# Performance work log

Measured on AMD Instinct MI355X. Metric: run time of the kernel, lower is better.

## Reference

```python
import jax, jax.numpy as jnp
import numpy as np

B, L, D, H, K_DELAYS = 8, 2048, 512, 8, 8
DH = D // H


def setup_inputs() -> dict:
    key = jax.random.key(0)
    ks = jax.random.split(key, 6)
    def lin_w(k):
        return 0.02 * jax.random.normal(k, (D, D), jnp.float32)
    return {
        "x_q":  jax.random.normal(ks[0], (B, L, D), jnp.float32),
        "x_kv": jax.random.normal(ks[1], (B, L, D), jnp.float32),
        "Wq": lin_w(ks[2]), "bq": jnp.zeros((D,), jnp.float32),
        "Wk": lin_w(ks[3]), "bk": jnp.zeros((D,), jnp.float32),
        "Wv": lin_w(ks[4]), "bv": jnp.zeros((D,), jnp.float32),
        "Wo": lin_w(ks[5]), "bo": jnp.zeros((D,), jnp.float32),
    }


def reference(x_q, x_kv, Wq, bq, Wk, bk, Wv, bv, Wo, bo):
    Bx, Lx, Dx = x_q.shape

    def proj(x, W, b):  # torch Linear: x @ W.T + b, then split heads -> [B,H,L,dh]
        return (x @ W.T + b).reshape(Bx, Lx, H, DH).transpose(0, 2, 1, 3)

    q = proj(x_q, Wq, bq)
    k = proj(x_kv, Wk, bk)
    v = proj(x_kv, Wv, bv)

    # FFT-based autocorrelation over the time axis (axis=2)
    qz = q - q.mean(axis=2, keepdims=True)
    kz = k - k.mean(axis=2, keepdims=True)
    Qf = jnp.fft.rfft(qz, axis=2)
    Kf = jnp.fft.rfft(kz, axis=2)
    corr = jnp.fft.irfft(Qf * jnp.conj(Kf), n=Lx, axis=2).mean(axis=-1)  # [B,H,L]
    # torch expands corr to [B,H,Lq,Lk] then means over Lq -> identical to corr
    score = corr

    K = min(K_DELAYS, Lx)
    vals, idx = jax.lax.top_k(score, K)                    # [B,H,K]
    w = vals / (vals.sum(axis=-1, keepdims=True) + 1e-12)
    w = jax.lax.stop_gradient(w)                           # .detach() in torch

    # circular shift by -delay == gather at (t + delay) mod L
    t = jnp.arange(Lx)
    pos = (t[None, None, None, :] + idx[..., None]) % Lx   # [B,H,K,L]
    v_sh = jnp.take_along_axis(v[:, :, None, :, :], pos[..., None], axis=3)  # [B,H,K,L,dh]
    out = jnp.einsum('bhk,bhkld->bhld', w, v_sh)           # weighted sum over delays

    out = out.transpose(0, 2, 1, 3).reshape(Bx, Lx, Dx)
    return out @ Wo.T + bo
```

## Files before the change

kernel.cpp:

```cpp
#include <hip/hip_runtime.h>
#include <math.h>

#define BB 8
#define LL 2048
#define DD 512
#define HH 8
#define DHH 64
#define KD 8
#define MM (BB*LL)

typedef _Float16 f16x2 __attribute__((ext_vector_type(2)));
typedef _Float16 f16x4 __attribute__((ext_vector_type(4)));
typedef _Float16 f16x8 __attribute__((ext_vector_type(8)));
typedef float    f32x4 __attribute__((ext_vector_type(4)));

__device__ inline void cvt8(const float* __restrict__ s, _Float16* hp, _Float16* lp) {
    const float4 a = *(const float4*)s;
    const float4 b = *(const float4*)(s + 4);
    const float v[8] = {a.x, a.y, a.z, a.w, b.x, b.y, b.z, b.w};
    f16x8 hi, lo;
#pragma unroll
    for (int j = 0; j < 8; j++) {
        const _Float16 h = (_Float16)v[j];
        hi[j] = h;
        lo[j] = (_Float16)((v[j] - (float)h) * 512.0f);
    }
    *(f16x8*)hp = hi;
    if (lp) *(f16x8*)lp = lo;
}

__global__ __launch_bounds__(256) void prep_all(const float* __restrict__ xq,
                                                const float* __restrict__ xkv,
                                                const float* __restrict__ Wq, const float* __restrict__ Wk,
                                                const float* __restrict__ Wv, const float* __restrict__ Wo,
                                                _Float16* __restrict__ Xq_h, _Float16* __restrict__ Xq_l,
                                                _Float16* __restrict__ Xkv_h, _Float16* __restrict__ Xkv_l,
                                                _Float16* __restrict__ Wq_h, _Float16* __restrict__ Wq_l,
                                                _Float16* __restrict__ Wk_h, _Float16* __restrict__ Wk_l,
                                                _Float16* __restrict__ Wv_h, _Float16* __restrict__ Wo_h) {
    const int bid = blockIdx.x;
    if (bid < 8192) {
        const int g = bid * 256 + threadIdx.x;
        const int which = g >> 20;
        const size_t idx = (size_t)(g & 1048575) * 8;
        const float* src = which ? xkv : xq;
        _Float16* dh = which ? Xkv_h : Xq_h;
        _Float16* dl = which ? Xkv_l : Xq_l;
        cvt8(src + idx, dh + idx, dl + idx);
    } else {
        const int g = (bid - 8192) * 256 + threadIdx.x;
        const int which = g >> 15;
        const size_t idx = (size_t)(g & 32767) * 8;
        if (which == 0)      cvt8(Wq + idx, Wq_h + idx, Wq_l + idx);
        else if (which == 1) cvt8(Wk + idx, Wk_h + idx, Wk_l + idx);
        else if (which == 2) cvt8(Wv + idx, Wv_h + idx, nullptr);
        else                 cvt8(Wo + idx, Wo_h + idx, nullptr);
    }
}

template<int NPROD, int MODE>
__device__ __forceinline__ void gemm_body(const _Float16* __restrict__ Ag,
                                          const _Float16* __restrict__ Al_g,
                                          const _Float16* __restrict__ Bg,
                                          const _Float16* __restrict__ Bl_g,
                                          const float* __restrict__ bias,
                                          void* __restrict__ Cv,
                                          _Float16* lds, int l0) {
    _Float16* Ah = lds;
    _Float16* Bh = lds + 5120;
    _Float16* Al = (NPROD == 3) ? lds + 10240 : lds;
    _Float16* Bl = (NPROD == 3) ? lds + 15360 : lds;

    const int t  = threadIdx.x;
    const int m0 = (((l0 >> 5) << 3) | (l0 & 7)) * 128;
    const int n0 = ((l0 >> 3) & 3) * 128;

    const int lrow = t >> 2;
    const int lcol = (t & 3) * 8;
    const int wave = t >> 6;
    const int lane = t & 63;
    const int wm   = (wave >> 1) * 64;
    const int wn   = (wave & 1) * 64;
    const int lm   = lane & 15;
    const int quad = lane >> 4;

    f32x4 acc0[4][4] = {};
    f32x4 acc1[4][4] = {};

    f16x8 pa[2], pb[2], pal[2], pbl[2];
#pragma unroll
    for (int p = 0; p < 2; p++) {
        pa[p] = *(const f16x8*)(Ag + (size_t)(m0 + p * 64 + lrow) * 512 + lcol);
        pb[p] = *(const f16x8*)(Bg + (size_t)(n0 + p * 64 + lrow) * 512 + lcol);
        if (NPROD == 3) {
            pal[p] = *(const f16x8*)(Al_g + (size_t)(m0 + p * 64 + lrow) * 512 + lcol);
            pbl[p] = *(const f16x8*)(Bl_g + (size_t)(n0 + p * 64 + lrow) * 512 + lcol);
        }
    }

    for (int k0 = 0; k0 < 512; k0 += 32) {
        __syncthreads();
#pragma unroll
        for (int p = 0; p < 2; p++) {
            const int row = p * 64 + lrow;
            *(f16x8*)&Ah[row * 40 + lcol] = pa[p];
            *(f16x8*)&Bh[row * 40 + lcol] = pb[p];
            if (NPROD == 3) {
                *(f16x8*)&Al[row * 40 + lcol] = pal[p];
                *(f16x8*)&Bl[row * 40 + lcol] = pbl[p];
            }
        }
        __syncthreads();

        if (k0 + 32 < 512) {
            const int kn = k0 + 32;
#pragma unroll
            for (int p = 0; p < 2; p++) {
                pa[p] = *(const f16x8*)(Ag + (size_t)(m0 + p * 64 + lrow) * 512 + kn + lcol);
                pb[p] = *(const f16x8*)(Bg + (size_t)(n0 + p * 64 + lrow) * 512 + kn + lcol);
                if (NPROD == 3) {
                    pal[p] = *(const f16x8*)(Al_g + (size_t)(m0 + p * 64 + lrow) * 512 + kn + lcol);
                    pbl[p] = *(const f16x8*)(Bl_g + (size_t)(n0 + p * 64 + lrow) * 512 + kn + lcol);
                }
            }
        }

        f16x8 afh[4], bf[4];
#pragma unroll
        for (int mt = 0; mt < 4; mt++)
            afh[mt] = *(f16x8*)&Ah[(wm + mt * 16 + lm) * 40 + quad * 8];
#pragma unroll
        for (int nt = 0; nt < 4; nt++)
            bf[nt] = *(f16x8*)&Bh[(wn + nt * 16 + lm) * 40 + quad * 8];

#pragma unroll
        for (int mt = 0; mt < 4; mt++)
#pragma unroll
            for (int nt = 0; nt < 4; nt++)
                acc0[mt][nt] = __builtin_amdgcn_mfma_f32_16x16x32_f16(afh[mt], bf[nt], acc0[mt][nt], 0, 0, 0);

        if (NPROD == 3) {
            f16x8 afl[4];
#pragma unroll
            for (int mt = 0; mt < 4; mt++)
                afl[mt] = *(f16x8*)&Al[(wm + mt * 16 + lm) * 40 + quad * 8];
#pragma unroll
            for (int mt = 0; mt < 4; mt++)
#pragma unroll
                for (int nt = 0; nt < 4; nt++)
                    acc1[mt][nt] = __builtin_amdgcn_mfma_f32_16x16x32_f16(afl[mt], bf[nt], acc1[mt][nt], 0, 0, 0);
#pragma unroll
            for (int nt = 0; nt < 4; nt++)
                bf[nt] = *(f16x8*)&Bl[(wn + nt * 16 + lm) * 40 + quad * 8];
#pragma unroll
            for (int mt = 0; mt < 4; mt++)
#pragma unroll
                for (int nt = 0; nt < 4; nt++)
                    acc1[mt][nt] = __builtin_amdgcn_mfma_f32_16x16x32_f16(afh[mt], bf[nt], acc1[mt][nt], 0, 0, 0);
        }
    }

#pragma unroll
    for (int mt = 0; mt < 4; mt++) {
#pragma unroll
        for (int nt = 0; nt < 4; nt++) {
            const int n = n0 + wn + nt * 16 + lm;
            const float bv = bias[n];
            float val[4];
#pragma unroll
            for (int r = 0; r < 4; r++) {
                val[r] = acc0[mt][nt][r] + bv;
                if (NPROD == 3) val[r] += acc1[mt][nt][r] * (1.0f / 512.0f);
            }
            const int mbase = m0 + wm + mt * 16 + quad * 4;
            const int b_idx = mbase >> 11;
            const int lbase = mbase & 2047;
            if (MODE == 0) {
                float* C = (float*)Cv;
#pragma unroll
                for (int r = 0; r < 4; r++) C[(size_t)(mbase + r) * 512 + n] = val[r];
            } else if (MODE == 1) {
                float* C = (float*)Cv;
                float4 pv = make_float4(val[0], val[1], val[2], val[3]);
                *(float4*)&C[((size_t)(b_idx * 512 + n)) * 2048 + lbase] = pv;
            } else {
                _Float16* C = (_Float16*)Cv;
#pragma unroll
                for (int r = 0; r < 4; r++)
                    C[(size_t)b_idx * 1048576 + (size_t)(n >> 6) * 131072
                      + (size_t)(lbase + r) * 64 + (n & 63)] = (_Float16)val[r];
            }
        }
    }
}

__global__ __launch_bounds__(256, 2) void gemm_qk(const _Float16* __restrict__ A0h, const _Float16* __restrict__ A0l,
                                                  const _Float16* __restrict__ B0h, const _Float16* __restrict__ B0l,
                                                  const float* __restrict__ bias0, float* __restrict__ C0,
                                                  const _Float16* __restrict__ A1h, const _Float16* __restrict__ A1l,
                                                  const _Float16* __restrict__ B1h, const _Float16* __restrict__ B1l,
                                                  const float* __restrict__ bias1, float* __restrict__ C1) {
    __shared__ __align__(16) _Float16 lds[20480];
    const int prob = blockIdx.x >> 9;
    const int l0   = blockIdx.x & 511;
    if (prob == 0)
        gemm_body<3, 1>(A0h, A0l, B0h, B0l, bias0, C0, lds, l0);
    else
        gemm_body<3, 1>(A1h, A1l, B1h, B1l, bias1, C1, lds, l0);
}

__global__ __launch_bounds__(256, 2) void gemm_v(const _Float16* __restrict__ Ah_g,
                                                 const _Float16* __restrict__ Bh_g,
                                                 const float* __restrict__ bias,
                                                 _Float16* __restrict__ C) {
    __shared__ __align__(16) _Float16 lds[10240];
    gemm_body<1, 2>(Ah_g, Ah_g, Bh_g, Bh_g, bias, C, lds, blockIdx.x);
}

__global__ __launch_bounds__(256, 2) void gemm_o(const _Float16* __restrict__ Ah_g,
                                                 const _Float16* __restrict__ Bh_g,
                                                 const float* __restrict__ bias,
                                                 float* __restrict__ C) {
    __shared__ __align__(16) _Float16 lds[10240];
    gemm_body<1, 0>(Ah_g, Ah_g, Bh_g, Bh_g, bias, C, lds, blockIdx.x);
}

#define PAD3(i) ((i) + ((i) >> 3))

__device__ inline float2 cmul2(float2 a, float2 w) {
    return make_float2(a.x * w.x - a.y * w.y, a.x * w.y + a.y * w.x);
}
__device__ inline float2 cadd2(float2 a, float2 b) { return make_float2(a.x + b.x, a.y + b.y); }
__device__ inline float2 csub2(float2 a, float2 b) { return make_float2(a.x - b.x, a.y - b.y); }

__global__ __launch_bounds__(256) void fft_fwd(const float* __restrict__ qT,
                                               const float* __restrict__ kT,
                                               float* __restrict__ specP) {
    const int blk  = blockIdx.x;
    const int bh   = blk >> 4;
    const int part = blk & 15;
    const int t    = threadIdx.x;
    __shared__ float2 Zs[2304];
    __shared__ float2 Wt[1024];

#pragma unroll
    for (int s = 0; s < 4; s++) {
        const int j = t + s * 256;
        float sv, cv;
        __sincosf(2.0f * (float)M_PI * (float)j / 2048.0f, &sv, &cv);
        Wt[j] = make_float2(cv, -sv);
    }

    float2 pacc[8];
#pragma unroll
    for (int s = 0; s < 8; s++) pacc[s] = make_float2(0.0f, 0.0f);

    const int low5 = t & 31, hi3 = t >> 5;
    const int low2 = t & 3,  hi6 = t >> 2;

    for (int j4 = 0; j4 < 4; j4++) {
        const int seq = bh * 64 + part * 4 + j4;
        const float* qp = qT + (size_t)seq * 2048;
        const float* kp = kT + (size_t)seq * 2048;
        float2 z[8];
#pragma unroll
        for (int s = 0; s < 8; s++) z[s] = make_float2(qp[t + 256 * s], kp[t + 256 * s]);
        __syncthreads();

#pragma unroll
        for (int sp = 0; sp < 4; sp++) {
            float2 u = z[sp], v = z[sp + 4];
            z[sp]     = cadd2(u, v);
            z[sp + 4] = cmul2(csub2(u, v), Wt[t + 256 * sp]);
        }
#pragma unroll
        for (int base = 0; base < 8; base += 4)
#pragma unroll
            for (int q2 = 0; q2 < 2; q2++) {
                float2 u = z[base + q2], v = z[base + q2 + 2];
                z[base + q2]     = cadd2(u, v);
                z[base + q2 + 2] = cmul2(csub2(u, v), Wt[2 * (t + 256 * q2)]);
            }
        {
            const float2 w = Wt[4 * t];
#pragma unroll
            for (int e = 0; e < 8; e += 2) {
                float2 u = z[e], v = z[e + 1];
                z[e]     = cadd2(u, v);
                z[e + 1] = cmul2(csub2(u, v), w);
            }
        }

#pragma unroll
        for (int s = 0; s < 8; s++) Zs[PAD3(t + 256 * s)] = z[s];
        __syncthreads();
#pragma unroll
        for (int s = 0; s < 8; s++) z[s] = Zs[PAD3(low5 + 32 * s + 256 * hi3)];

#pragma unroll
        for (int sp = 0; sp < 4; sp++) {
            float2 u = z[sp], v = z[sp + 4];
            z[sp]     = cadd2(u, v);
            z[sp + 4] = cmul2(csub2(u, v), Wt[8 * (low5 + 32 * sp)]);
        }
#pragma unroll
        for (int base = 0; base < 8; base += 4)
#pragma unroll
            for (int q2 = 0; q2 < 2; q2++) {
                float2 u = z[base + q2], v = z[base + q2 + 2];
                z[base + q2]     = cadd2(u, v);
                z[base + q2 + 2] = cmul2(csub2(u, v), Wt[16 * (low5 + 32 * q2)]);
            }
        {
            const float2 w = Wt[32 * low5];
#pragma unroll
            for (int e = 0; e < 8; e += 2) {
                float2 u = z[e], v = z[e + 1];
                z[e]     = cadd2(u, v);
                z[e + 1] = cmul2(csub2(u, v), w);
            }
        }

#pragma unroll
        for (int s = 0; s < 8; s++) Zs[PAD3(low5 + 32 * s + 256 * hi3)] = z[s];
        __syncthreads();
#pragma unroll
        for (int s = 0; s < 8; s++) z[s] = Zs[PAD3(low2 + 4 * s + 32 * hi6)];

#pragma unroll
        for (int sp = 0; sp < 4; sp++) {
            float2 u = z[sp], v = z[sp + 4];
            z[sp]     = cadd2(u, v);
            z[sp + 4] = cmul2(csub2(u, v), Wt[64 * (low2 + 4 * sp)]);
        }
#pragma unroll
        for (int base = 0; base < 8; base += 4)
#pragma unroll
            for (int q2 = 0; q2 < 2; q2++) {
                float2 u = z[base + q2], v = z[base + q2 + 2];
                z[base + q2]     = cadd2(u, v);
                z[base + q2 + 2] = cmul2(csub2(u, v), Wt[128 * (low2 + 4 * q2)]);
            }
        {
            const float2 w = Wt[256 * low2];
#pragma unroll
            for (int e = 0; e < 8; e += 2) {
                float2 u = z[e], v = z[e + 1];
                z[e]     = cadd2(u, v);
                z[e + 1] = cmul2(csub2(u, v), w);
            }
        }

#pragma unroll
        for (int s = 0; s < 8; s++) Zs[PAD3(low2 + 4 * s + 32 * hi6)] = z[s];
        __syncthreads();
#pragma unroll
        for (int s = 0; s < 8; s++) z[s] = Zs[PAD3(8 * t + s)];

#pragma unroll
        for (int base = 0; base < 8; base += 4) {
            {
                float2 u = z[base], v = z[base + 2];
                z[base]     = cadd2(u, v);
                z[base + 2] = csub2(u, v);
            }
            {
                float2 u = z[base + 1], v = z[base + 3];
                float2 d = csub2(u, v);
                z[base + 1] = cadd2(u, v);
                z[base + 3] = make_float2(d.y, -d.x);
            }
        }
#pragma unroll
        for (int e = 0; e < 8; e += 2) {
            float2 u = z[e], v = z[e + 1];
            z[e]     = cadd2(u, v);
            z[e + 1] = csub2(u, v);
        }

#pragma unroll
        for (int s = 0; s < 8; s++) Zs[PAD3(8 * t + s)] = z[s];
        __syncthreads();

#pragma unroll
        for (int s = 0; s < 8; s++) {
            const int p  = t + 256 * s;
            const int f  = (int)(__brev((unsigned)p) >> 21);
            const int fm = (2048 - f) & 2047;
            const int p2 = (int)(__brev((unsigned)fm) >> 21);
            const float2 zf = Zs[PAD3(p)];
            const float2 zm = Zs[PAD3(p2)];
            const float qr = 0.5f * (zf.x + zm.x);
            const float qi = 0.5f * (zf.y - zm.y);
            const float kr = 0.5f * (zf.y + zm.y);
            const float ki = 0.5f * (zm.x - zf.x);
            if (f != 0) {
                pacc[s].x += qr * kr + qi * ki;
                pacc[s].y += qi * kr - qr * ki;
            }
        }
    }

    float2* outp = (float2*)specP + (size_t)blk * 2048;
#pragma unroll
    for (int s = 0; s < 8; s++) outp[t + 256 * s] = pacc[s];
}

__device__ inline void build_twiddle(float2* Wt, int tid, float sign) {
#pragma unroll
    for (int s = 0; s < 4; s++) {
        const int j = tid + s * 256;
        const float a = 2.0f * (float)M_PI * (float)j / 2048.0f;
        float sv, cv;
        __sincosf(a, &sv, &cv);
        Wt[j] = make_float2(cv, sign * sv);
    }
}

__device__ inline void fft2048_stages(float2* Z, const float2* Wt, int tid) {
    for (int st = 0; st < 11; st++) {
        const int half = 1 << st;
        const int shift = 10 - st;
#pragma unroll
        for (int r = 0; r < 4; r++) {
            const int m   = tid + r * 256;
            const int grp = m >> st;
            const int pos = m & (half - 1);
            const int i0  = (grp << (st + 1)) + pos;
            const int i1  = i0 + half;
            const float2 w = Wt[pos << shift];
            const float2 a = Z[i0];
            const float2 b = Z[i1];
            const float tr = b.x * w.x - b.y * w.y;
            const float ti = b.x * w.y + b.y * w.x;
            Z[i0] = make_float2(a.x + tr, a.y + ti);
            Z[i1] = make_float2(a.x - tr, a.y - ti);
        }
        __syncthreads();
    }
}

__global__ __launch_bounds__(256) void fft_inv_topk(const float* __restrict__ specP,
                                                    int* __restrict__ delays,
                                                    float* __restrict__ weights) {
    const int bh  = blockIdx.x;
    const int tid = threadIdx.x;
    __shared__ float2 Z[2048];
    __shared__ float2 Wt[1024];
    __shared__ float  corrS[2048];
    __shared__ float  rv[256];
    __shared__ int    ri[256];
    __shared__ float  vals[KD];
    __shared__ int    inds[KD];

    build_twiddle(Wt, tid, +1.0f);

    const float2* sp = (const float2*)specP + (size_t)bh * 16 * 2048;
#pragma unroll
    for (int s = 0; s < 8; s++) {
        const int p = tid + s * 256;
        float2 acc = make_float2(0.0f, 0.0f);
#pragma unroll
        for (int part = 0; part < 16; part++) {
            const float2 v = sp[part * 2048 + p];
            acc.x += v.x; acc.y += v.y;
        }
        Z[p] = acc;
    }
    __syncthreads();
    fft2048_stages(Z, Wt, tid);

    const float scale = 1.0f / (2048.0f * 64.0f);
#pragma unroll
    for (int s = 0; s < 8; s++) {
        const int i = tid + s * 256;
        corrS[i] = Z[i].x * scale;
    }
    __syncthreads();

    for (int k = 0; k < KD; k++) {
        float best = -1e30f;
        int   bi   = 1 << 30;
        for (int i = tid; i < 2048; i += 256) {
            const float v = corrS[i];
            if (v > best || (v == best && i < bi)) { best = v; bi = i; }
        }
        rv[tid] = best;
        ri[tid] = bi;
        __syncthreads();
        for (int off = 128; off > 0; off >>= 1) {
            if (tid < off) {
                const float v2 = rv[tid + off];
                const int   i2 = ri[tid + off];
                if (v2 > rv[tid] || (v2 == rv[tid] && i2 < ri[tid])) {
                    rv[tid] = v2; ri[tid] = i2;
                }
            }
            __syncthreads();
        }
        if (tid == 0) {
            vals[k] = rv[0];
            inds[k] = ri[0];
            corrS[ri[0]] = -1e30f;
        }
        __syncthreads();
    }

    if (tid == 0) {
        float sum = 0.0f;
        for (int k = 0; k < KD; k++) sum += vals[k];
        const float inv = 1.0f / (sum + 1e-12f);
        for (int k = 0; k < KD; k++) {
            weights[bh * KD + k] = vals[k] * inv;
            delays[bh * KD + k]  = inds[k];
        }
    }
}

__global__ __launch_bounds__(256) void gather_ws(const _Float16* __restrict__ v,
                                                 const int* __restrict__ delays,
                                                 const float* __restrict__ weights,
                                                 _Float16* __restrict__ outb) {
    const int gp = blockIdx.x * 256 + threadIdx.x;
    const int c8 = gp & 63;
    const int m  = gp >> 6;
    const int l  = m & 2047;
    const int b  = m >> 11;
    const int ch = c8 * 8;
    const int h  = ch >> 6;
    const int dh = ch & 63;
    const int bh = b * 8 + h;

    const _Float16* vb = v + (size_t)bh * 131072;
    float a[8] = {};
#pragma unroll
    for (int k = 0; k < KD; k++) {
        const int   d = delays[bh * KD + k];
        const float w = weights[bh * KD + k];
        const int   p = (l + d) & 2047;
        const f16x8 pv = *(const f16x8*)&vb[p * 64 + dh];
#pragma unroll
        for (int j = 0; j < 8; j++) a[j] = fmaf(w, (float)pv[j], a[j]);
    }
    f16x8 ov;
#pragma unroll
    for (int j = 0; j < 8; j++) ov[j] = (_Float16)a[j];
    *(f16x8*)&outb[(size_t)m * 512 + ch] = ov;
}

extern "C" void kernel_launch(void* const* d_in, const int* in_sizes, int n_in,
                              void* d_out, int out_size, void* d_ws, size_t ws_size,
                              hipStream_t stream) {
    const float* x_q  = (const float*)d_in[0];
    const float* x_kv = (const float*)d_in[1];
    const float* Wq   = (const float*)d_in[2];
    const float* bq   = (const float*)d_in[3];
    const float* Wk   = (const float*)d_in[4];
    const float* bk   = (const float*)d_in[5];
    const float* Wv   = (const float*)d_in[6];
    const float* bv   = (const float*)d_in[7];
    const float* Wo   = (const float*)d_in[8];
    const float* bo   = (const float*)d_in[9];
    float* out = (float*)d_out;

    char* ws = (char*)d_ws;
    _Float16* Xq_h  = (_Float16*)(ws + 0);
    _Float16* Xq_l  = (_Float16*)(ws + 16777216);
    _Float16* Xkv_h = (_Float16*)(ws + 33554432);
    _Float16* Xkv_l = (_Float16*)(ws + 50331648);
    _Float16* Wq_h  = (_Float16*)(ws + 67108864);
    _Float16* Wq_l  = (_Float16*)(ws + 67633152);
    _Float16* Wk_h  = (_Float16*)(ws + 68157440);
    _Float16* Wk_l  = (_Float16*)(ws + 68681728);
    _Float16* Wv_h  = (_Float16*)(ws + 69206016);
    _Float16* Wo_h  = (_Float16*)(ws + 69730304);
    int*      dely  = (int*)    (ws + 70254592);
    float*    wgt   = (float*)  (ws + 70256640);
    float*    kf32  = (float*)  (ws + 75497472);
    float*    specP = (float*)  (ws + 50331648);
    _Float16* vh    = (_Float16*)(ws + 0);
    _Float16* gbuf  = (_Float16*)(ws + 16777216);
    float*    qf32  = (float*)d_out;

    (void)0;

    dim3 blk(256);

    prep_all<<<dim3(8704), blk, 0, stream>>>(x_q, x_kv, Wq, Wk, Wv, Wo,
                                             Xq_h, Xq_l, Xkv_h, Xkv_l,
                                             Wq_h, Wq_l, Wk_h, Wk_l, Wv_h, Wo_h);

    gemm_qk<<<dim3(512), blk, 0, stream>>>(Xq_h, Xq_l, Wq_h, Wq_l, bq, qf32,
                                           Xq_h, Xq_l, Wq_h, Wq_l, bq, qf32);
    {
        float* kf32_ = (float*)(ws + 0);
        gemm_qk<<<dim3(512), blk, 0, stream>>>(Xkv_h, Xkv_l, Wk_h, Wk_l, bk, kf32_,
                                               Xkv_h, Xkv_l, Wk_h, Wk_l, bk, kf32_);
    }

    fft_fwd<<<dim3(1024), blk, 0, stream>>>(qf32, (float*)(ws + 0), specP);
    fft_inv_topk<<<dim3(BB * HH), blk, 0, stream>>>(specP, dely, wgt);

    gemm_v<<<dim3(512), blk, 0, stream>>>(Xkv_h, Wv_h, bv, vh);

    gather_ws<<<dim3(4096), blk, 0, stream>>>(vh, dely, wgt, gbuf);

    gemm_o<<<dim3(512), blk, 0, stream>>>(gbuf, Wo_h, bo, out);
}
```

Measured before the change: 302.3 us.

## Merge inverse FFT/top-k into V-projection GEMM launch and use wave-shuffle top-k

Combines the 64-block inverse-FFT/top-k kernel with the V-projection GEMM into one 576-block launch: the first 64 blocks do the FFT path and the rest do GEMM tiles, so the small, latency-bound FFT work overlaps with the GEMM instead of running alone on a mostly idle GPU. The top-k selection now keeps correlation values in registers and reduces with wavefront shuffles plus a 4-entry cross-wave step, replacing the shared-memory tree reduction that needed many barriers per iteration. Shared memory is a single raw buffer sized for the larger of the two uses, which may reduce occupancy for the GEMM blocks.

```diff
diff --git a/kernel.cpp b/kernel.cpp
--- a/kernel.cpp
+++ b/kernel.cpp
@@ -209,14 +209,6 @@
         gemm_body<3, 1>(A1h, A1l, B1h, B1l, bias1, C1, lds, l0);
 }
 
-__global__ __launch_bounds__(256, 2) void gemm_v(const _Float16* __restrict__ Ah_g,
-                                                 const _Float16* __restrict__ Bh_g,
-                                                 const float* __restrict__ bias,
-                                                 _Float16* __restrict__ C) {
-    __shared__ __align__(16) _Float16 lds[10240];
-    gemm_body<1, 2>(Ah_g, Ah_g, Bh_g, Bh_g, bias, C, lds, blockIdx.x);
-}
-
 __global__ __launch_bounds__(256, 2) void gemm_o(const _Float16* __restrict__ Ah_g,
                                                  const _Float16* __restrict__ Bh_g,
                                                  const float* __restrict__ bias,
@@ -440,18 +432,27 @@
     }
 }
 
-__global__ __launch_bounds__(256) void fft_inv_topk(const float* __restrict__ specP,
-                                                    int* __restrict__ delays,
-                                                    float* __restrict__ weights) {
-    const int bh  = blockIdx.x;
+__global__ __launch_bounds__(256, 2) void gemm_v_fftinv(const _Float16* __restrict__ Ah_g,
+                                                        const _Float16* __restrict__ Bh_g,
+                                                        const float* __restrict__ bias,
+                                                        _Float16* __restrict__ C,
+                                                        const float* __restrict__ specP,
+                                                        int* __restrict__ delays,
+                                                        float* __restrict__ weights) {
+    __shared__ __align__(16) char smem[24608];
+    const int bid = blockIdx.x;
     const int tid = threadIdx.x;
-    __shared__ float2 Z[2048];
-    __shared__ float2 Wt[1024];
-    __shared__ float  corrS[2048];
-    __shared__ float  rv[256];
-    __shared__ int    ri[256];
-    __shared__ float  vals[KD];
-    __shared__ int    inds[KD];
+
+    if (bid >= 64) {
+        gemm_body<1, 2>(Ah_g, Ah_g, Bh_g, Bh_g, bias, C, (_Float16*)smem, bid - 64);
+        return;
+    }
+
+    const int bh = bid;
+    float2* Z  = (float2*)smem;
+    float2* Wt = (float2*)(smem + 16384);
+    float*  wv = (float*)(smem + 24576);
+    int*    wi = (int*)(smem + 24592);
 
     build_twiddle(Wt, tid, +1.0f);
 
@@ -471,48 +472,57 @@
     fft2048_stages(Z, Wt, tid);
 
     const float scale = 1.0f / (2048.0f * 64.0f);
-#pragma unroll
-    for (int s = 0; s < 8; s++) {
-        const int i = tid + s * 256;
-        corrS[i] = Z[i].x * scale;
-    }
-    __syncthreads();
-
+    float cv[8];
+#pragma unroll
+    for (int s = 0; s < 8; s++) cv[s] = Z[tid + s * 256].x * scale;
+
+    float bkv[KD];
+    int   bki[KD];
+#pragma unroll
     for (int k = 0; k < KD; k++) {
-        float best = -1e30f;
-        int   bi   = 1 << 30;
-        for (int i = tid; i < 2048; i += 256) {
-            const float v = corrS[i];
-            if (v > best || (v == best && i < bi)) { best = v; bi = i; }
-        }
-        rv[tid] = best;
-        ri[tid] = bi;
-        __syncthreads();
-        for (int off = 128; off > 0; off >>= 1) {
-            if (tid < off) {
-                const float v2 = rv[tid + off];
-                const int   i2 = ri[tid + off];
-                if (v2 > rv[tid] || (v2 == rv[tid] && i2 < ri[tid])) {
-                    rv[tid] = v2; ri[tid] = i2;
-                }
-            }
-            __syncthreads();
-        }
-        if (tid == 0) {
-            vals[k] = rv[0];
-            inds[k] = ri[0];
-            corrS[ri[0]] = -1e30f;
+        float lv = -1e30f;
+        int   li = 1 << 30;
+#pragma unroll
+        for (int s = 0; s < 8; s++) {
+            const int idx = tid + s * 256;
+            if (cv[s] > lv || (cv[s] == lv && idx < li)) { lv = cv[s]; li = idx; }
+        }
+#pragma unroll
+        for (int off = 1; off < 64; off <<= 1) {
+            const float v2 = __shfl_xor(lv, off);
+            const int   i2 = __shfl_xor(li, off);
+            if (v2 > lv || (v2 == lv && i2 < li)) { lv = v2; li = i2; }
+        }
+        if ((tid & 63) == 0) { wv[tid >> 6] = lv; wi[tid >> 6] = li; }
+        __syncthreads();
+        float bv = wv[0];
+        int   bi = wi[0];
+#pragma unroll
+        for (int j = 1; j < 4; j++) {
+            const float v2 = wv[j];
+            const int   i2 = wi[j];
+            if (v2 > bv || (v2 == bv && i2 < bi)) { bv = v2; bi = i2; }
+        }
+        bkv[k] = bv;
+        bki[k] = bi;
+        if ((bi & 255) == tid) {
+            const int slot = bi >> 8;
+#pragma unroll
+            for (int s = 0; s < 8; s++)
+                if (s == slot) cv[s] = -1e30f;
         }
         __syncthreads();
     }
 
     if (tid == 0) {
         float sum = 0.0f;
-        for (int k = 0; k < KD; k++) sum += vals[k];
+#pragma unroll
+        for (int k = 0; k < KD; k++) sum += bkv[k];
         const float inv = 1.0f / (sum + 1e-12f);
+#pragma unroll
         for (int k = 0; k < KD; k++) {
-            weights[bh * KD + k] = vals[k] * inv;
-            delays[bh * KD + k]  = inds[k];
+            weights[bh * KD + k] = bkv[k] * inv;
+            delays[bh * KD + k]  = bki[k];
         }
     }
 }
@@ -576,13 +586,10 @@
     _Float16* Wo_h  = (_Float16*)(ws + 69730304);
     int*      dely  = (int*)    (ws + 70254592);
     float*    wgt   = (float*)  (ws + 70256640);
-    float*    kf32  = (float*)  (ws + 75497472);
     float*    specP = (float*)  (ws + 50331648);
     _Float16* vh    = (_Float16*)(ws + 0);
     _Float16* gbuf  = (_Float16*)(ws + 16777216);
     float*    qf32  = (float*)d_out;
-
-    (void)0;
 
     dim3 blk(256);
 
@@ -599,9 +606,8 @@
     }
 
     fft_fwd<<<dim3(1024), blk, 0, stream>>>(qf32, (float*)(ws + 0), specP);
-    fft_inv_topk<<<dim3(BB * HH), blk, 0, stream>>>(specP, dely, wgt);
-
-    gemm_v<<<dim3(512), blk, 0, stream>>>(Xkv_h, Wv_h, bv, vh);
+
+    gemm_v_fftinv<<<dim3(576), blk, 0, stream>>>(Xkv_h, Wv_h, bv, vh, specP, dely, wgt);
 
     gather_ws<<<dim3(4096), blk, 0, stream>>>(vh, dely, wgt, gbuf);
 
```

Result: faster. 284.9 us (-5.8%).
